# Kernel tuning notes

Hardware: AMD Instinct MI355X
Metric: run time of the kernel (lower is better)

The kernel has to match this reference:

```python
import jax, jax.numpy as jnp
import numpy as np

B, C, S, H, W = 64, 768, 8, 28, 28

def setup_inputs() -> dict:
    key = jax.random.key(0)
    k1, k2, k3 = jax.random.split(key, 3)
    x = jax.random.normal(k1, (B, C, H, W), dtype=jnp.float32)
    # Conv2d(token_dim -> num_region, k=3, pad=1); torch default init scale ~ 1/sqrt(fan_in)
    fan_in = C * 3 * 3
    bound = 1.0 / np.sqrt(fan_in)
    conv_w = jax.random.uniform(k2, (S, C, 3, 3), dtype=jnp.float32, minval=-bound, maxval=bound)
    conv_b = jax.random.uniform(k3, (S,), dtype=jnp.float32, minval=-bound, maxval=bound)
    return {"x": x, "conv_w": conv_w, "conv_b": conv_b}

def reference(x, conv_w, conv_b):
    # spatial attention conv: [B,C,H,W] -> [B,S,H,W]
    region_mask = jax.lax.conv_general_dilated(
        x, conv_w, window_strides=(1, 1), padding=((1, 1), (1, 1)),
        dimension_numbers=("NCHW", "OIHW", "NCHW"))
    region_mask = region_mask + conv_b[None, :, None, None]
    # fused per-region weighted global average pooling:
    # for each region s: mean over HW of x * mask_s  ==> single batched contraction
    hw = x.shape[2] * x.shape[3]
    learned_regions = jnp.einsum("bchw,bshw->bcs", x, region_mask) / hw  # [B,C,S]
    return learned_regions, region_mask
```

## Files before the change

### kernel.cpp

```cpp
#include <hip/hip_runtime.h>

#define B_ 64
#define C_ 768
#define S_ 8
#define HW_ 784
#define CPB_ 48
#define NCHUNK_ 16

__global__ __launch_bounds__(256) void wtrans_k(
    const float* __restrict__ w, float* __restrict__ wT2)
{
  int idx = blockIdx.x * 256 + threadIdx.x;
  int c = idx / 72, r = idx - c * 72;
  int t = r / 8, s = r - t * 8;
  wT2[idx] = w[(size_t)s * (C_ * 9) + c * 9 + t];
}

__global__ __launch_bounds__(256) void conv_k(
    const float* __restrict__ x, const float* __restrict__ wT2,
    float* __restrict__ mask_acc)
{
  __shared__ float wl[CPB_ * 72];
  const int tid = threadIdx.x;
  const int c0  = blockIdx.y * CPB_;

  {
    const float4* wsrc = (const float4*)(wT2 + (size_t)c0 * 72);
    float4* wd = (float4*)wl;
    #pragma unroll
    for (int r = 0; r < 4; ++r) {
      int i = tid + r * 256;
      if (i < CPB_ * 18) wd[i] = wsrc[i];
    }
  }
  __syncthreads();

  const int flat = blockIdx.x * 256 + tid;
  const int b    = flat / 392;
  const int pr   = flat - b * 392;
  const int h2   = pr / 28;
  const int wI   = pr - h2 * 28;
  const int h    = h2 * 2;

  int ro[4]; float rm[4];
  #pragma unroll
  for (int dr = 0; dr < 4; ++dr) {
    int r = h - 1 + dr;
    rm[dr] = (r >= 0 && r < 28) ? 1.0f : 0.0f;
    ro[dr] = min(max(r, 0), 27) * 28;
  }
  int co[3]; float cm[3];
  #pragma unroll
  for (int dc = 0; dc < 3; ++dc) {
    int cc = wI - 1 + dc;
    cm[dc] = (cc >= 0 && cc < 28) ? 1.0f : 0.0f;
    co[dc] = min(max(cc, 0), 27);
  }
  int   eoff[12]; float msk[12];
  #pragma unroll
  for (int dr = 0; dr < 4; ++dr)
    #pragma unroll
    for (int dc = 0; dc < 3; ++dc) {
      eoff[dr * 3 + dc] = ro[dr] + co[dc];
      msk[dr * 3 + dc]  = rm[dr] * cm[dc];
    }

  float acc[2][S_];
  #pragma unroll
  for (int px = 0; px < 2; ++px)
    #pragma unroll
    for (int s = 0; s < S_; ++s) acc[px][s] = 0.0f;

  int xoff = (b * C_ + c0) * HW_;

  for (int cl = 0; cl < CPB_; ++cl, xoff += HW_) {
    float xv[12];
    #pragma unroll
    for (int t = 0; t < 12; ++t)
      xv[t] = x[xoff + eoff[t]] * msk[t];

    const float4* wrow = (const float4*)&wl[cl * 72];
    #pragma unroll
    for (int ky = 0; ky < 3; ++ky)
      #pragma unroll
      for (int kx = 0; kx < 3; ++kx) {
        const int t9 = ky * 3 + kx;
        float4 wa = wrow[t9 * 2];
        float4 wb = wrow[t9 * 2 + 1];
        float x0 = xv[ky * 3 + kx];
        float x1 = xv[(ky + 1) * 3 + kx];
        acc[0][0] = fmaf(x0, wa.x, acc[0][0]);
        acc[0][1] = fmaf(x0, wa.y, acc[0][1]);
        acc[0][2] = fmaf(x0, wa.z, acc[0][2]);
        acc[0][3] = fmaf(x0, wa.w, acc[0][3]);
        acc[0][4] = fmaf(x0, wb.x, acc[0][4]);
        acc[0][5] = fmaf(x0, wb.y, acc[0][5]);
        acc[0][6] = fmaf(x0, wb.z, acc[0][6]);
        acc[0][7] = fmaf(x0, wb.w, acc[0][7]);
        acc[1][0] = fmaf(x1, wa.x, acc[1][0]);
        acc[1][1] = fmaf(x1, wa.y, acc[1][1]);
        acc[1][2] = fmaf(x1, wa.z, acc[1][2]);
        acc[1][3] = fmaf(x1, wa.w, acc[1][3]);
        acc[1][4] = fmaf(x1, wb.x, acc[1][4]);
        acc[1][5] = fmaf(x1, wb.y, acc[1][5]);
        acc[1][6] = fmaf(x1, wb.z, acc[1][6]);
        acc[1][7] = fmaf(x1, wb.w, acc[1][7]);
      }
  }

  float* dst = mask_acc + (size_t)b * S_ * HW_ + h * 28 + wI;
  #pragma unroll
  for (int s = 0; s < S_; ++s)
    #pragma unroll
    for (int px = 0; px < 2; ++px)
      atomicAdd(dst + (size_t)s * HW_ + px * 28, acc[px][s]);
}

__global__ __launch_bounds__(256) void mask_bias_k(
    const float* __restrict__ mask_acc, const float* __restrict__ bias,
    float* __restrict__ outM)
{
  int i4 = blockIdx.x * 256 + threadIdx.x;
  float4 v = ((const float4*)mask_acc)[i4];
  int s = (i4 / 196) & 7;
  float bv = bias[s];
  v.x += bv; v.y += bv; v.z += bv; v.w += bv;
  ((float4*)outM)[i4] = v;
}

__global__ __launch_bounds__(256) void einsum_k(
    const float* __restrict__ x, const float* __restrict__ mask_acc,
    const float* __restrict__ bias, float* __restrict__ out)
{
  const int tid  = threadIdx.x;
  const int lane = tid & 63;
  const int wv   = tid >> 6;
  const int b    = blockIdx.y;
  const int c    = (blockIdx.x * 4 + wv) * 2;

  const float4* xr0 = (const float4*)(x + ((size_t)b * C_ + c) * HW_);
  const float4* xr1 = xr0 + 196;
  const float4* mr  = (const float4*)(mask_acc + (size_t)b * S_ * HW_);

  float a0[S_], a1[S_];
  #pragma unroll
  for (int s = 0; s < S_; ++s) { a0[s] = 0.0f; a1[s] = 0.0f; }
  float sx0 = 0.0f, sx1 = 0.0f;

  #pragma unroll
  for (int jf = 0; jf < 3; ++jf) {
    int j4 = jf * 64 + lane;
    float4 xa = xr0[j4];
    float4 xb = xr1[j4];
    sx0 += xa.x + xa.y + xa.z + xa.w;
    sx1 += xb.x + xb.y + xb.z + xb.w;
    #pragma unroll
    for (int s = 0; s < S_; ++s) {
      float4 m = mr[s * 196 + j4];
      a0[s] = fmaf(xa.x, m.x, fmaf(xa.y, m.y, fmaf(xa.z, m.z, fmaf(xa.w, m.w, a0[s]))));
      a1[s] = fmaf(xb.x, m.x, fmaf(xb.y, m.y, fmaf(xb.z, m.z, fmaf(xb.w, m.w, a1[s]))));
    }
  }
  if (lane < 4) {
    int j4 = 192 + lane;
    float4 xa = xr0[j4];
    float4 xb = xr1[j4];
    sx0 += xa.x + xa.y + xa.z + xa.w;
    sx1 += xb.x + xb.y + xb.z + xb.w;
    #pragma unroll
    for (int s = 0; s < S_; ++s) {
      float4 m = mr[s * 196 + j4];
      a0[s] = fmaf(xa.x, m.x, fmaf(xa.y, m.y, fmaf(xa.z, m.z, fmaf(xa.w, m.w, a0[s]))));
      a1[s] = fmaf(xb.x, m.x, fmaf(xb.y, m.y, fmaf(xb.z, m.z, fmaf(xb.w, m.w, a1[s]))));
    }
  }

  #pragma unroll
  for (int d = 1; d < 64; d <<= 1) {
    #pragma unroll
    for (int s = 0; s < S_; ++s) {
      a0[s] += __shfl_xor(a0[s], d, 64);
      a1[s] += __shfl_xor(a1[s], d, 64);
    }
    sx0 += __shfl_xor(sx0, d, 64);
    sx1 += __shfl_xor(sx1, d, 64);
  }

  if (lane == 0) {
    float* o = out + ((size_t)b * C_ + c) * S_;
    #pragma unroll
    for (int s = 0; s < S_; ++s) {
      o[s]      = (a0[s] + bias[s] * sx0) * (1.0f / HW_);
      o[S_ + s] = (a1[s] + bias[s] * sx1) * (1.0f / HW_);
    }
  }
}

extern "C" void kernel_launch(void* const* d_in, const int* in_sizes, int n_in,
                              void* d_out, int out_size, void* d_ws, size_t ws_size,
                              hipStream_t stream) {
  const float* x    = (const float*)d_in[0];
  const float* w    = (const float*)d_in[1];
  const float* bias = (const float*)d_in[2];
  float* out  = (float*)d_out;
  float* outM = out + (size_t)B_ * C_ * S_;
  float* acc  = (float*)d_ws;
  float* wT2  = acc + (size_t)B_ * S_ * HW_;

  hipMemsetAsync(acc, 0, (size_t)B_ * S_ * HW_ * sizeof(float), stream);
  wtrans_k<<<(C_ * 72) / 256, 256, 0, stream>>>(w, wT2);
  conv_k<<<dim3(98, NCHUNK_), 256, 0, stream>>>(x, wT2, acc);
  mask_bias_k<<<(B_ * S_ * HW_ / 4 + 255) / 256, 256, 0, stream>>>(acc, bias, outM);
  einsum_k<<<dim3(96, B_), 256, 0, stream>>>(x, acc, bias, out);
}
```

Measured before the change: 334.6 us.

## Compute conv via bf16x3-split MFMA with padded LDS input tiles

```diff
diff --git a/kernel.cpp b/kernel.cpp
--- a/kernel.cpp
+++ b/kernel.cpp
@@ -1,119 +1,138 @@
 #include <hip/hip_runtime.h>
+
+typedef __attribute__((ext_vector_type(8))) short short8;
+typedef __attribute__((ext_vector_type(4))) float f32x4;
 
 #define B_ 64
 #define C_ 768
 #define S_ 8
 #define HW_ 784
-#define CPB_ 48
-#define NCHUNK_ 16
+#define NQ_ 4
+#define KSPLIT_ 3
+#define KCH_ 256
+#define NKS_ 8
+#define PP_ 330
+#define FS_ 40
 
 __global__ __launch_bounds__(256) void wtrans_k(
-    const float* __restrict__ w, float* __restrict__ wT2)
+    const float* __restrict__ w, unsigned short* __restrict__ wpack)
 {
   int idx = blockIdx.x * 256 + threadIdx.x;
-  int c = idx / 72, r = idx - c * 72;
-  int t = r / 8, s = r - t * 8;
-  wT2[idx] = w[(size_t)s * (C_ * 9) + c * 9 + t];
+  int c   = idx % C_;
+  int col = (idx / C_) & 15;
+  int t   = idx / (C_ * 16);
+  int s   = col & 7;
+  float wv = w[(size_t)s * (C_ * 9) + c * 9 + t];
+  unsigned u = __builtin_bit_cast(unsigned, wv);
+  unsigned short hi = (unsigned short)(u >> 16);
+  float r = wv - __builtin_bit_cast(float, u & 0xffff0000u);
+  unsigned short lo = (unsigned short)(__builtin_bit_cast(unsigned, r) >> 16);
+  wpack[idx] = (col < 8) ? hi : lo;
 }
 
 __global__ __launch_bounds__(256) void conv_k(
-    const float* __restrict__ x, const float* __restrict__ wT2,
+    const float* __restrict__ x, const unsigned short* __restrict__ wpack,
     float* __restrict__ mask_acc)
 {
-  __shared__ float wl[CPB_ * 72];
-  const int tid = threadIdx.x;
-  const int c0  = blockIdx.y * CPB_;
-
-  {
-    const float4* wsrc = (const float4*)(wT2 + (size_t)c0 * 72);
-    float4* wd = (float4*)wl;
-    #pragma unroll
-    for (int r = 0; r < 4; ++r) {
-      int i = tid + r * 256;
-      if (i < CPB_ * 18) wd[i] = wsrc[i];
-    }
-  }
-  __syncthreads();
-
-  const int flat = blockIdx.x * 256 + tid;
-  const int b    = flat / 392;
-  const int pr   = flat - b * 392;
-  const int h2   = pr / 28;
-  const int wI   = pr - h2 * 28;
-  const int h    = h2 * 2;
-
-  int ro[4]; float rm[4];
-  #pragma unroll
-  for (int dr = 0; dr < 4; ++dr) {
-    int r = h - 1 + dr;
-    rm[dr] = (r >= 0 && r < 28) ? 1.0f : 0.0f;
-    ro[dr] = min(max(r, 0), 27) * 28;
-  }
-  int co[3]; float cm[3];
-  #pragma unroll
-  for (int dc = 0; dc < 3; ++dc) {
-    int cc = wI - 1 + dc;
-    cm[dc] = (cc >= 0 && cc < 28) ? 1.0f : 0.0f;
-    co[dc] = min(max(cc, 0), 27);
-  }
-  int   eoff[12]; float msk[12];
-  #pragma unroll
-  for (int dr = 0; dr < 4; ++dr)
-    #pragma unroll
-    for (int dc = 0; dc < 3; ++dc) {
-      eoff[dr * 3 + dc] = ro[dr] + co[dc];
-      msk[dr * 3 + dc]  = rm[dr] * cm[dc];
-    }
-
-  float acc[2][S_];
-  #pragma unroll
-  for (int px = 0; px < 2; ++px)
-    #pragma unroll
-    for (int s = 0; s < S_; ++s) acc[px][s] = 0.0f;
-
-  int xoff = (b * C_ + c0) * HW_;
-
-  for (int cl = 0; cl < CPB_; ++cl, xoff += HW_) {
-    float xv[12];
-    #pragma unroll
-    for (int t = 0; t < 12; ++t)
-      xv[t] = x[xoff + eoff[t]] * msk[t];
-
-    const float4* wrow = (const float4*)&wl[cl * 72];
-    #pragma unroll
-    for (int ky = 0; ky < 3; ++ky)
+  __shared__ unsigned short fh[PP_ * FS_];
+  __shared__ unsigned short fl[PP_ * FS_];
+  const int tid  = threadIdx.x;
+  const int lane = tid & 63;
+  const int wv   = tid >> 6;
+  const int b    = blockIdx.x;
+  const int q    = blockIdx.y;
+  const int cz   = blockIdx.z * KCH_;
+  const int col  = lane & 15;
+  const int cg   = lane >> 4;
+
+  for (int i = tid; i < PP_ * FS_ / 2; i += 256) {
+    ((unsigned*)fh)[i] = 0u; ((unsigned*)fl)[i] = 0u;
+  }
+
+  int ppt[4], tb[4], ntile = 0;
+  #pragma unroll
+  for (int i = 0; i < 4; ++i) {
+    int tl = wv + i * 4;
+    if (tl < 13) {
+      int pl = tl * 16 + col;
+      int h = pl / 28, wc = pl - h * 28;
+      ppt[i] = (h + 1) * 30 + wc + 1;
+      tb[i]  = tl * 16;
+      ntile  = i + 1;
+    }
+  }
+
+  f32x4 acc[4];
+  #pragma unroll
+  for (int i = 0; i < 4; ++i) acc[i] = (f32x4){0.f, 0.f, 0.f, 0.f};
+
+  for (int ks = 0; ks < NKS_; ++ks) {
+    const int c0 = cz + ks * 32;
+    __syncthreads();
+    #pragma unroll
+    for (int it = 0; it < 4; ++it) {
+      int i = tid + it * 256;
+      if (i < 1008) {
+        int cp = i / 63, rem = i - cp * 63;
+        int r = rem / 7, c4 = rem - r * 7;
+        int gr = q * 7 - 1 + r;
+        if (gr >= 0 && gr < 28) {
+          float4 va = ((const float4*)x)[(size_t)(b * C_ + c0 + 2 * cp) * 196 + gr * 7 + c4];
+          float4 vb = ((const float4*)x)[(size_t)(b * C_ + c0 + 2 * cp + 1) * 196 + gr * 7 + c4];
+          #pragma unroll
+          for (int j = 0; j < 4; ++j) {
+            int pp = r * 30 + c4 * 4 + j + 1;
+            float a = ((const float*)&va)[j], bb = ((const float*)&vb)[j];
+            unsigned ua = __builtin_bit_cast(unsigned, a);
+            unsigned ub = __builtin_bit_cast(unsigned, bb);
+            float ra = a  - __builtin_bit_cast(float, ua & 0xffff0000u);
+            float rb = bb - __builtin_bit_cast(float, ub & 0xffff0000u);
+            unsigned la = __builtin_bit_cast(unsigned, ra) >> 16;
+            unsigned lb = __builtin_bit_cast(unsigned, rb) >> 16;
+            ((unsigned*)fh)[pp * 20 + cp] = (ua >> 16) | ((ub >> 16) << 16);
+            ((unsigned*)fl)[pp * 20 + cp] = la | (lb << 16);
+          }
+        }
+      }
+    }
+    short8 bf[9];
+    #pragma unroll
+    for (int t = 0; t < 9; ++t)
+      bf[t] = *(const short8*)(wpack + (size_t)(t * 16 + col) * C_ + c0 + cg * 8);
+    __syncthreads();
+
+    #pragma unroll
+    for (int i = 0; i < 4; ++i) {
+      if (i < ntile) {
+        const int base = ppt[i] * FS_ + cg * 8;
+        #pragma unroll
+        for (int dy = -1; dy <= 1; ++dy)
+          #pragma unroll
+          for (int dx = -1; dx <= 1; ++dx) {
+            int off = base + (dy * 30 + dx) * FS_;
+            short8 ah = *(const short8*)(fh + off);
+            short8 al = *(const short8*)(fl + off);
+            int t = (dy + 1) * 3 + (dx + 1);
+            acc[i] = __builtin_amdgcn_mfma_f32_16x16x32_bf16(ah, bf[t], acc[i], 0, 0, 0);
+            acc[i] = __builtin_amdgcn_mfma_f32_16x16x32_bf16(al, bf[t], acc[i], 0, 0, 0);
+          }
+      }
+    }
+  }
+
+  #pragma unroll
+  for (int i = 0; i < 4; ++i) {
+    if (i < ntile) {
       #pragma unroll
-      for (int kx = 0; kx < 3; ++kx) {
-        const int t9 = ky * 3 + kx;
-        float4 wa = wrow[t9 * 2];
-        float4 wb = wrow[t9 * 2 + 1];
-        float x0 = xv[ky * 3 + kx];
-        float x1 = xv[(ky + 1) * 3 + kx];
-        acc[0][0] = fmaf(x0, wa.x, acc[0][0]);
-        acc[0][1] = fmaf(x0, wa.y, acc[0][1]);
-        acc[0][2] = fmaf(x0, wa.z, acc[0][2]);
-        acc[0][3] = fmaf(x0, wa.w, acc[0][3]);
-        acc[0][4] = fmaf(x0, wb.x, acc[0][4]);
-        acc[0][5] = fmaf(x0, wb.y, acc[0][5]);
-        acc[0][6] = fmaf(x0, wb.z, acc[0][6]);
-        acc[0][7] = fmaf(x0, wb.w, acc[0][7]);
-        acc[1][0] = fmaf(x1, wa.x, acc[1][0]);
-        acc[1][1] = fmaf(x1, wa.y, acc[1][1]);
-        acc[1][2] = fmaf(x1, wa.z, acc[1][2]);
-        acc[1][3] = fmaf(x1, wa.w, acc[1][3]);
-        acc[1][4] = fmaf(x1, wb.x, acc[1][4]);
-        acc[1][5] = fmaf(x1, wb.y, acc[1][5]);
-        acc[1][6] = fmaf(x1, wb.z, acc[1][6]);
-        acc[1][7] = fmaf(x1, wb.w, acc[1][7]);
+      for (int r4 = 0; r4 < 4; ++r4) {
+        float v = acc[i][r4];
+        v += __shfl_xor(v, 8, 64);
+        int pl = tb[i] + cg * 4 + r4;
+        if (col < 8 && pl < 196)
+          atomicAdd(mask_acc + ((size_t)b * S_ + col) * HW_ + q * 196 + pl, v);
       }
-  }
-
-  float* dst = mask_acc + (size_t)b * S_ * HW_ + h * 28 + wI;
-  #pragma unroll
-  for (int s = 0; s < S_; ++s)
-    #pragma unroll
-    for (int px = 0; px < 2; ++px)
-      atomicAdd(dst + (size_t)s * HW_ + px * 28, acc[px][s]);
+    }
+  }
 }
 
 __global__ __launch_bounds__(256) void mask_bias_k(
@@ -205,11 +224,11 @@
   float* out  = (float*)d_out;
   float* outM = out + (size_t)B_ * C_ * S_;
   float* acc  = (float*)d_ws;
-  float* wT2  = acc + (size_t)B_ * S_ * HW_;
+  unsigned short* wpack = (unsigned short*)(acc + (size_t)B_ * S_ * HW_);
 
   hipMemsetAsync(acc, 0, (size_t)B_ * S_ * HW_ * sizeof(float), stream);
-  wtrans_k<<<(C_ * 72) / 256, 256, 0, stream>>>(w, wT2);
-  conv_k<<<dim3(98, NCHUNK_), 256, 0, stream>>>(x, wT2, acc);
+  wtrans_k<<<(9 * 16 * C_) / 256, 256, 0, stream>>>(w, wpack);
+  conv_k<<<dim3(B_, NQ_, KSPLIT_), 256, 0, stream>>>(x, wpack, acc);
   mask_bias_k<<<(B_ * S_ * HW_ / 4 + 255) / 256, 256, 0, stream>>>(acc, bias, outM);
   einsum_k<<<dim3(96, B_), 256, 0, stream>>>(x, acc, bias, out);
 }
```

Result: faster. 295.2 us (-11.8%).
